# Kernel tuning notes

Measured on AMD Instinct MI355X. Metric: run time of the kernel, lower is better.

Reference implementation:

```python
import jax, jax.numpy as jnp
import numpy as np

TAU = 0.25
VTH = 1.0
RESET = 0.0


def setup_inputs() -> dict:
    key = jax.random.key(0)
    B, T, U = 64, 256, 1024
    inputs = jax.random.normal(key, (B, T, U), dtype=jnp.float32)
    return {"inputs": inputs}


def reference(inputs):
    # inputs: (B, T, U). LIF recurrence over time with threshold + soft reset.
    dt = inputs.dtype
    tau = jnp.asarray(TAU, dt)
    vth = jnp.asarray(VTH, dt)
    reset = jnp.asarray(RESET, dt)

    def step(v, x_t):
        v = tau * v + (1.0 - tau) * x_t          # leaky integrate
        s = (v > vth).astype(dt)                  # fire
        v = v - s * vth + s * reset               # reset fired neurons
        return v, s

    B, T, U = inputs.shape
    v0 = jnp.zeros((B, U), dtype=dt)
    xs = jnp.swapaxes(inputs, 0, 1)               # (T, B, U)
    _, spikes = jax.lax.scan(step, v0, xs)        # (T, B, U)
    return jnp.swapaxes(spikes, 0, 1)             # (B, T, U)
```

## Files before the change

kernel.cpp:

```cpp
#include <hip/hip_runtime.h>
#include <hip/hip_bf16.h>


constexpr int kB = 64;
constexpr int kT = 256;
constexpr int kU = 1024;

__global__ __launch_bounds__(256)
void lif_kernel(const float* __restrict__ x, float* __restrict__ out) {
    const int idx = blockIdx.x * blockDim.x + threadIdx.x;
    const int b = idx / kU;
    const int u = idx - b * kU;

    const size_t base = (size_t)b * kT * kU + u;
    const float* __restrict__ xp = x + base;
    float* __restrict__ op = out + base;

    float v = 0.0f;
#pragma unroll 8
    for (int t = 0; t < kT; ++t) {
        const float xt = xp[(size_t)t * kU];
        const float a = __fmul_rn(0.25f, v);
        const float c = __fmul_rn(0.75f, xt);
        v = __fadd_rn(a, c);
        const float s = (v > 1.0f) ? 1.0f : 0.0f;
        v = __fsub_rn(v, s);
        op[(size_t)t * kU] = s;
    }
}

extern "C" void kernel_launch(void* const* d_in, const int* in_sizes, int n_in,
                              void* d_out, int out_size, void* d_ws, size_t ws_size,
                              hipStream_t stream) {
    const float* x = (const float*)d_in[0];
    float* out = (float*)d_out;

    const int nthreads = kB * kU;
    const int block = 256;
    const int grid = nthreads / block;
    lif_kernel<<<grid, block, 0, stream>>>(x, out);
}
```

Baseline: 131.1 us.

## Software-pipeline input loads in chunks of 16 and use nontemporal spike stores

Restructures the time loop into chunks of 16 steps, prefetching the next chunk's inputs into registers while the current chunk is computed. This keeps more loads in flight per thread to hide memory latency in the serial recurrence. Output stores become nontemporal so streamed spikes do not pollute cache. It costs extra registers (two buffers of 16 floats), which could reduce occupancy.

```diff
diff --git a/kernel.cpp b/kernel.cpp
--- a/kernel.cpp
+++ b/kernel.cpp
@@ -5,27 +5,52 @@
 constexpr int kB = 64;
 constexpr int kT = 256;
 constexpr int kU = 1024;
+constexpr int kC = 16;
 
 __global__ __launch_bounds__(256)
 void lif_kernel(const float* __restrict__ x, float* __restrict__ out) {
     const int idx = blockIdx.x * blockDim.x + threadIdx.x;
-    const int b = idx / kU;
-    const int u = idx - b * kU;
+    const int b = idx >> 10;
+    const int u = idx & (kU - 1);
 
     const size_t base = (size_t)b * kT * kU + u;
     const float* __restrict__ xp = x + base;
     float* __restrict__ op = out + base;
 
+    float buf[kC];
+#pragma unroll
+    for (int j = 0; j < kC; ++j)
+        buf[j] = xp[(size_t)j * kU];
+
     float v = 0.0f;
-#pragma unroll 8
-    for (int t = 0; t < kT; ++t) {
-        const float xt = xp[(size_t)t * kU];
+    for (int c = 0; c < kT / kC - 1; ++c) {
+        const int t0 = c * kC;
+        float nbuf[kC];
+#pragma unroll
+        for (int j = 0; j < kC; ++j)
+            nbuf[j] = xp[(size_t)(t0 + kC + j) * kU];
+#pragma unroll
+        for (int j = 0; j < kC; ++j) {
+            const float a = __fmul_rn(0.25f, v);
+            const float cc = __fmul_rn(0.75f, buf[j]);
+            v = __fadd_rn(a, cc);
+            const float s = (v > 1.0f) ? 1.0f : 0.0f;
+            v = __fsub_rn(v, s);
+            __builtin_nontemporal_store(s, &op[(size_t)(t0 + j) * kU]);
+        }
+#pragma unroll
+        for (int j = 0; j < kC; ++j)
+            buf[j] = nbuf[j];
+    }
+    const int t0 = kT - kC;
+#pragma unroll
+    for (int j = 0; j < kC; ++j) {
         const float a = __fmul_rn(0.25f, v);
-        const float c = __fmul_rn(0.75f, xt);
-        v = __fadd_rn(a, c);
+        const float cc = __fmul_rn(0.75f, buf[j]);
+        v = __fadd_rn(a, cc);
         const float s = (v > 1.0f) ? 1.0f : 0.0f;
         v = __fsub_rn(v, s);
-        op[(size_t)t * kU] = s;
+        __builtin_nontemporal_store(s, &op[(size_t)(t0 + j) * kU]);
     }
 }
 
```

Result: faster. 109.4 us (-16.6%).

## Prefetch input in register groups and stage spikes through LDS for vector stores

Applied to the files above, without the earlier changes.

Inputs are now loaded in groups of 16 timesteps, with the next group prefetched into registers while the current group is computed. This keeps more loads in flight to hide memory latency. Spike outputs for each wave go to a padded shared-memory tile and are written back as 16-byte nontemporal vector stores, replacing scalar strided stores. The cost is more registers, LDS traffic and a reliance on wave-level LDS ordering without explicit barriers.

```diff
diff --git a/kernel.cpp b/kernel.cpp
--- a/kernel.cpp
+++ b/kernel.cpp
@@ -2,30 +2,66 @@
 #include <hip/hip_bf16.h>
 
 
+typedef float vfloat4 __attribute__((ext_vector_type(4)));
+
 constexpr int kB = 64;
 constexpr int kT = 256;
 constexpr int kU = 1024;
+constexpr int kG = 16;
+constexpr int kPad = 72;
 
 __global__ __launch_bounds__(256)
 void lif_kernel(const float* __restrict__ x, float* __restrict__ out) {
-    const int idx = blockIdx.x * blockDim.x + threadIdx.x;
-    const int b = idx / kU;
-    const int u = idx - b * kU;
+    const int idx  = blockIdx.x * blockDim.x + threadIdx.x;
+    const int b    = idx >> 10;
+    const int u    = idx & (kU - 1);
+    const int lane = threadIdx.x & 63;
+    const int wav  = threadIdx.x >> 6;
 
     const size_t base = (size_t)b * kT * kU + u;
     const float* __restrict__ xp = x + base;
-    float* __restrict__ op = out + base;
+    const int ubase = u - lane;
+    const size_t obase = (size_t)b * kT * kU + ubase;
+
+    __shared__ float tile[4][kG][kPad];
+    float (*T)[kPad] = tile[wav];
+
+    float buf[kG], nbuf[kG];
+#pragma unroll
+    for (int j = 0; j < kG; ++j)
+        buf[j] = xp[(size_t)j * kU];
 
     float v = 0.0f;
-#pragma unroll 8
-    for (int t = 0; t < kT; ++t) {
-        const float xt = xp[(size_t)t * kU];
-        const float a = __fmul_rn(0.25f, v);
-        const float c = __fmul_rn(0.75f, xt);
-        v = __fadd_rn(a, c);
-        const float s = (v > 1.0f) ? 1.0f : 0.0f;
-        v = __fsub_rn(v, s);
-        op[(size_t)t * kU] = s;
+    for (int g = 0; g < kT / kG; ++g) {
+        const int t0 = g * kG;
+        const bool more = (g + 1 < kT / kG);
+        if (more) {
+#pragma unroll
+            for (int j = 0; j < kG; ++j)
+                nbuf[j] = xp[(size_t)(t0 + kG + j) * kU];
+        }
+#pragma unroll
+        for (int j = 0; j < kG; ++j) {
+            const float a  = __fmul_rn(0.25f, v);
+            const float cc = __fmul_rn(0.75f, buf[j]);
+            v = __fadd_rn(a, cc);
+            const float s = (v > 1.0f) ? 1.0f : 0.0f;
+            v = __fsub_rn(v, s);
+            T[j][lane] = s;
+        }
+#pragma unroll
+        for (int p = 0; p < 4; ++p) {
+            const int tt  = lane & 15;
+            const int grp = (lane >> 4) + 4 * p;
+            const vfloat4 w = *(const vfloat4*)&T[tt][grp * 4];
+            __builtin_nontemporal_store(
+                w, (vfloat4*)&out[obase + (size_t)(t0 + tt) * kU + grp * 4]);
+        }
+        if (more) {
+#pragma unroll
+            for (int j = 0; j < kG; ++j)
+                buf[j] = nbuf[j];
+        }
     }
 }
 
```

Result: faster. 113.1 us (-13.7%).
